# Optimization experiments

Hardware: AMD Instinct MI355X
Metric: run time of the kernel (lower is better)

Reference implementation:

```python
import jax, jax.numpy as jnp
import numpy as np

D_MODEL = 1024
D_STATE = 16
D_CONV = 4
EXPAND = 2
D_INNER = D_MODEL * EXPAND
B_BATCH = 2
SEQ_L = 2048


def setup_inputs() -> dict:
    key = jax.random.key(0)
    ks = jax.random.split(key, 9)
    x = jax.random.normal(ks[0], (B_BATCH, SEQ_L, D_MODEL), dtype=jnp.float32)
    # Parameters (torch nn.Linear stores weight as (out, in))
    in_proj_w = jax.random.normal(ks[1], (2 * D_INNER, D_MODEL), jnp.float32) / np.sqrt(D_MODEL)
    conv_w = jax.random.normal(ks[2], (D_INNER, 1, D_CONV), jnp.float32) / np.sqrt(D_CONV)
    conv_b = jax.random.normal(ks[3], (D_INNER,), jnp.float32) * 0.01
    dt_w = jax.random.normal(ks[4], (D_INNER, D_INNER), jnp.float32) / np.sqrt(D_INNER)
    dt_b = jax.random.uniform(ks[5], (D_INNER,), jnp.float32, 1.0, 2.0)
    B_proj_w = jax.random.normal(ks[6], (D_STATE, D_INNER), jnp.float32) / np.sqrt(D_INNER)
    C_proj_w = jax.random.normal(ks[7], (D_STATE, D_INNER), jnp.float32) / np.sqrt(D_INNER)
    A_log = jnp.broadcast_to(jnp.log(jnp.linspace(1.0, D_STATE, D_STATE, dtype=jnp.float32))[None, :], (D_INNER, D_STATE)).copy()
    D_param = jnp.ones((D_INNER,), jnp.float32)
    out_proj_w = jax.random.normal(ks[8], (D_MODEL, D_INNER), jnp.float32) / np.sqrt(D_INNER)
    return {"x": x, "in_proj_w": in_proj_w, "conv_w": conv_w, "conv_b": conv_b,
            "dt_w": dt_w, "dt_b": dt_b, "B_proj_w": B_proj_w, "C_proj_w": C_proj_w,
            "A_log": A_log, "D_param": D_param, "out_proj_w": out_proj_w}


def reference(x, in_proj_w, conv_w, conv_b, dt_w, dt_b, B_proj_w, C_proj_w, A_log, D_param, out_proj_w):
    Bb, L, _ = x.shape
    # 1. input projection + split into (x_proj, z)
    xz = jnp.einsum('bld,ed->ble', x, in_proj_w)            # (B, L, 2*Din)
    x_p, z = jnp.split(xz, 2, axis=-1)                      # each (B, L, Din)
    # 2. causal depthwise conv1d (left-pad K-1, trim to L == torch pad=K-1 then [:L])
    xc = x_p.transpose(0, 2, 1)                             # (B, Din, L)
    K = conv_w.shape[-1]
    xc = jax.lax.conv_general_dilated(xc, conv_w, window_strides=(1,),
                                      padding=[(K - 1, 0)],
                                      feature_group_count=xc.shape[1])
    xc = xc + conv_b[None, :, None]
    xs = jax.nn.silu(xc).transpose(0, 2, 1)                 # (B, L, Din)
    # 3. SSM parameter projections
    dt = jax.nn.softplus(jnp.einsum('bld,ed->ble', xs, dt_w) + dt_b)  # (B, L, Din)
    Bp = jnp.einsum('bld,nd->bln', xs, B_proj_w)            # (B, L, N)
    Cp = jnp.einsum('bld,nd->bln', xs, C_proj_w)            # (B, L, N)
    A = -jnp.exp(A_log)                                     # (Din, N)
    # 4. selective scan: h[t] = exp(dt*A)*h[t-1] + dt*B*x ; y = <h, C> + D*x
    def step(h, inp):
        dt_t, B_t, x_t, C_t = inp                           # (B,Din),(B,N),(B,Din),(B,N)
        a = jnp.exp(dt_t[..., None] * A)                    # (B, Din, N)
        b = dt_t[..., None] * B_t[:, None, :] * x_t[..., None]
        h = a * h + b
        y_t = jnp.einsum('bdn,bn->bd', h, C_t)
        return h, y_t
    h0 = jnp.zeros((Bb, xs.shape[-1], A.shape[1]), x.dtype)
    scan_in = (dt.transpose(1, 0, 2), Bp.transpose(1, 0, 2),
               xs.transpose(1, 0, 2), Cp.transpose(1, 0, 2))
    _, ys = jax.lax.scan(step, h0, scan_in)                 # (L, B, Din)
    y = ys.transpose(1, 0, 2) + D_param * xs                # (B, L, Din)
    # 5. gated output projection
    y = y * jax.nn.silu(z)
    return jnp.einsum('ble,de->bld', y, out_proj_w)         # (B, L, d_model)
```

## Files before the change

### kernel.cpp

```cpp
#include <hip/hip_runtime.h>
#include <cmath>

#define BB 2
#define LL 2048
#define DMODEL 1024
#define DIN 2048
#define NST 16
#define NC 32
#define TC 64

typedef short short8 __attribute__((ext_vector_type(8)));
typedef float f32x4 __attribute__((ext_vector_type(4)));
typedef unsigned short u16;

__device__ __forceinline__ float bf2f(u16 u) {
    union { unsigned u; float f; } v; v.u = ((unsigned)u) << 16; return v.f;
}
__device__ __forceinline__ u16 f2bf(float f) {
    union { float f; unsigned u; } v; v.f = f;
    unsigned r = v.u + 0x7FFFu + ((v.u >> 16) & 1u);
    return (u16)(r >> 16);
}

__global__ __launch_bounds__(256) void cvt_bf16(const float* __restrict__ in,
                                                u16* __restrict__ out) {
    int i = (blockIdx.x * 256 + threadIdx.x) * 4;
    float4 v = *reinterpret_cast<const float4*>(in + i);
    ushort4 o = {f2bf(v.x), f2bf(v.y), f2bf(v.z), f2bf(v.w)};
    *reinterpret_cast<ushort4*>(out + i) = o;
}

template <int KDIM, int EPI>
__global__ __launch_bounds__(256, 2) void gemm128(const u16* __restrict__ A,
                                                  const u16* __restrict__ B,
                                                  void* __restrict__ Cout, int N,
                                                  const float* __restrict__ bias,
                                                  float* __restrict__ Bp,
                                                  float* __restrict__ Cp) {
    constexpr int NT = KDIM / 64;
    __shared__ u16 lds[32768];
    const int tid = threadIdx.x;
    const int lane = tid & 63;
    const int wave = tid >> 6;
    const int bm = blockIdx.y * 128;
    const int bn = blockIdx.x * 128;
    const int wr = (wave >> 1) * 64;
    const int wc = (wave & 1) * 64;
    const int fr = lane & 15;
    const int kg8 = (lane >> 4) * 8;

    u16* const A0 = lds;
    u16* const B0 = lds + 8192;
    u16* const A1 = lds + 16384;
    u16* const B1 = lds + 24576;

    f32x4 acc[4][4];
#pragma unroll
    for (int i = 0; i < 4; ++i)
#pragma unroll
        for (int j = 0; j < 4; ++j) acc[i][j] = (f32x4){0.f, 0.f, 0.f, 0.f};

    auto STAGE = [&](const u16* __restrict__ G, int br, int kt, u16* dst) {
#pragma unroll
        for (int rr = 0; rr < 4; ++rr) {
            int c = rr * 256 + tid;
            int cs = c ^ ((c >> 4) & 7);
            __builtin_amdgcn_global_load_lds(
                (const __attribute__((address_space(1))) void*)(
                    G + (size_t)(br + (cs >> 3)) * KDIM + kt + ((cs & 7) << 3)),
                (__attribute__((address_space(3))) void*)(dst + c * 8), 16, 0, 0);
        }
    };
    auto LDSW = [&](const u16* tile, int row, int k) -> short8 {
        int u = row * 64 + k;
        u ^= ((u >> 7) & 7) << 3;
        return *reinterpret_cast<const short8*>(tile + u);
    };

    STAGE(A, bm, 0, A0);
    STAGE(B, bn, 0, B0);
    __syncthreads();

#pragma unroll 1
    for (int t = 0; t < NT; ++t) {
        const u16* const Ac = (t & 1) ? A1 : A0;
        const u16* const Bc = (t & 1) ? B1 : B0;
        u16* const An = (t & 1) ? A0 : A1;
        u16* const Bn = (t & 1) ? B0 : B1;

        if (t + 1 < NT) {
            STAGE(A, bm, (t + 1) * 64, An);
            STAGE(B, bn, (t + 1) * 64, Bn);
        }

        short8 af[4][2], bf[4][2];
#pragma unroll
        for (int f = 0; f < 4; ++f)
#pragma unroll
            for (int ks = 0; ks < 2; ++ks)
                af[f][ks] = LDSW(Ac, wr + f * 16 + fr, ks * 32 + kg8);
#pragma unroll
        for (int j = 0; j < 4; ++j)
#pragma unroll
            for (int ks = 0; ks < 2; ++ks)
                bf[j][ks] = LDSW(Bc, wc + j * 16 + fr, ks * 32 + kg8);

#pragma unroll
        for (int ks = 0; ks < 2; ++ks)
#pragma unroll
            for (int f = 0; f < 4; ++f)
#pragma unroll
                for (int j = 0; j < 4; ++j)
                    acc[f][j] = __builtin_amdgcn_mfma_f32_16x16x32_bf16(
                        af[f][ks], bf[j][ks], acc[f][j], 0, 0, 0);

        __syncthreads();
    }

    const int crow0 = (lane >> 4) * 4;
    const int ccol = lane & 15;
#pragma unroll
    for (int f = 0; f < 4; ++f)
#pragma unroll
        for (int j = 0; j < 4; ++j) {
            const int col = bn + wc + j * 16 + ccol;
            if (EPI == 1 && col >= DIN + 32) continue;
            float bv = (EPI == 1 && col < DIN) ? bias[col] : 0.f;
#pragma unroll
            for (int r = 0; r < 4; ++r) {
                const int row = bm + wr + f * 16 + crow0 + r;
                float v = acc[f][j][r];
                if (EPI == 0) {
                    ((float*)Cout)[(size_t)row * N + col] = v;
                } else if (EPI == 2) {
                    ((u16*)Cout)[(size_t)row * N + col] = f2bf(v);
                } else {
                    if (col < DIN) {
                        v += bv;
                        v = (v > 20.0f) ? v : log1pf(__expf(v));
                        ((float*)Cout)[(size_t)row * DIN + col] = v;
                    } else if (col < DIN + 16) {
                        Bp[(size_t)row * NST + (col - DIN)] = v;
                    } else {
                        Cp[(size_t)row * NST + (col - DIN - 16)] = v;
                    }
                }
            }
        }
}

__global__ __launch_bounds__(256) void conv_silu(const u16* __restrict__ xz,
                                                 const float* __restrict__ w,
                                                 const float* __restrict__ b,
                                                 u16* __restrict__ xsb) {
    int idx = blockIdx.x * 256 + threadIdx.x;
    int d = idx & (DIN - 1);
    int t = (idx >> 11) & (LL - 1);
    int bb = idx >> 22;
    const u16* xp = xz + (size_t)bb * LL * 4096;
    float acc = b[d];
#pragma unroll
    for (int k = 0; k < 4; ++k) {
        int tt = t - 3 + k;
        if (tt >= 0) acc = fmaf(w[d * 4 + k], bf2f(xp[(size_t)tt * 4096 + d]), acc);
    }
    float s = acc / (1.0f + __expf(-acc));
    xsb[idx] = f2bf(s);
}

__global__ __launch_bounds__(256) void scan1(const float* __restrict__ dt,
                                             const u16* __restrict__ xs,
                                             const float* __restrict__ Bp,
                                             const float* __restrict__ A_log,
                                             float* __restrict__ aprod,
                                             float* __restrict__ hout) {
    const int db = blockIdx.x & 7;
    const int c = (blockIdx.x >> 3) & (NC - 1);
    const int b = blockIdx.x >> 8;
    const int d = db * 256 + threadIdx.x;
    const int t0 = c * TC;

    __shared__ float Bs[TC * NST];
    for (int i = threadIdx.x; i < TC * NST; i += 256)
        Bs[i] = Bp[((size_t)b * LL + t0) * NST + i];
    __syncthreads();

    float Ac[NST];
#pragma unroll
    for (int n = 0; n < NST; ++n) Ac[n] = -__expf(A_log[d * NST + n]);

    float ap[NST], h[NST];
#pragma unroll
    for (int n = 0; n < NST; ++n) { ap[n] = 1.0f; h[n] = 0.0f; }

    const float* dtp = dt + ((size_t)b * LL + t0) * DIN + d;
    const u16*  xp  = xs + ((size_t)b * LL + t0) * DIN + d;

    for (int tt = 0; tt < TC; ++tt) {
        float dtv = dtp[(size_t)tt * DIN];
        float xv = bf2f(xp[(size_t)tt * DIN]);
        float bx = dtv * xv;
#pragma unroll
        for (int n = 0; n < NST; ++n) {
            float a = __expf(dtv * Ac[n]);
            ap[n] *= a;
            h[n] = fmaf(a, h[n], bx * Bs[tt * NST + n]);
        }
    }
#pragma unroll
    for (int n = 0; n < NST; ++n) {
        size_t idx = (((size_t)(b * NC + c) * NST) + n) * DIN + d;
        aprod[idx] = ap[n];
        hout[idx] = h[n];
    }
}

__global__ __launch_bounds__(256) void scan2(const float* __restrict__ aprod,
                                             const float* __restrict__ hout,
                                             float* __restrict__ hin) {
    const int gid = blockIdx.x * 256 + threadIdx.x;
    const int d = gid & (DIN - 1);
    const int n = (gid >> 11) & (NST - 1);
    const int b = gid >> 15;
    float h = 0.0f;
    for (int c = 0; c < NC; ++c) {
        size_t idx = (((size_t)(b * NC + c) * NST) + n) * DIN + d;
        hin[idx] = h;
        h = fmaf(aprod[idx], h, hout[idx]);
    }
}

__global__ __launch_bounds__(256) void scan3(const float* __restrict__ dt,
                                             const u16* __restrict__ xs,
                                             const u16* __restrict__ xz,
                                             const float* __restrict__ Bp,
                                             const float* __restrict__ Cp,
                                             const float* __restrict__ hin,
                                             const float* __restrict__ A_log,
                                             const float* __restrict__ Dp,
                                             u16* __restrict__ ybf) {
    const int db = blockIdx.x & 7;
    const int c = (blockIdx.x >> 3) & (NC - 1);
    const int b = blockIdx.x >> 8;
    const int d = db * 256 + threadIdx.x;
    const int t0 = c * TC;

    __shared__ float Bs[TC * NST];
    __shared__ float Cs[TC * NST];
    for (int i = threadIdx.x; i < TC * NST; i += 256) {
        Bs[i] = Bp[((size_t)b * LL + t0) * NST + i];
        Cs[i] = Cp[((size_t)b * LL + t0) * NST + i];
    }
    __syncthreads();

    float Ac[NST], h[NST];
#pragma unroll
    for (int n = 0; n < NST; ++n) {
        Ac[n] = -__expf(A_log[d * NST + n]);
        h[n] = hin[(((size_t)(b * NC + c) * NST) + n) * DIN + d];
    }
    const float Dv = Dp[d];

    const float* dtp = dt + ((size_t)b * LL + t0) * DIN + d;
    const u16*  xp  = xs + ((size_t)b * LL + t0) * DIN + d;
    const u16*  zp  = xz + ((size_t)b * LL + t0) * 4096 + DIN + d;
    u16* yp = ybf + ((size_t)b * LL + t0) * DIN + d;

    for (int tt = 0; tt < TC; ++tt) {
        float dtv = dtp[(size_t)tt * DIN];
        float xv = bf2f(xp[(size_t)tt * DIN]);
        float zv = bf2f(zp[(size_t)tt * 4096]);
        float bx = dtv * xv;
        float y = 0.0f;
#pragma unroll
        for (int n = 0; n < NST; ++n) {
            float a = __expf(dtv * Ac[n]);
            h[n] = fmaf(a, h[n], bx * Bs[tt * NST + n]);
            y = fmaf(h[n], Cs[tt * NST + n], y);
        }
        y = fmaf(Dv, xv, y);
        float g = zv / (1.0f + __expf(-zv));
        yp[(size_t)tt * DIN] = f2bf(y * g);
    }
}

extern "C" void kernel_launch(void* const* d_in, const int* in_sizes, int n_in,
                              void* d_out, int out_size, void* d_ws, size_t ws_size,
                              hipStream_t stream) {
    const float* x          = (const float*)d_in[0];
    const float* in_proj_w  = (const float*)d_in[1];
    const float* conv_w     = (const float*)d_in[2];
    const float* conv_b     = (const float*)d_in[3];
    const float* dt_w       = (const float*)d_in[4];
    const float* dt_b       = (const float*)d_in[5];
    const float* B_proj_w   = (const float*)d_in[6];
    const float* C_proj_w   = (const float*)d_in[7];
    const float* A_log      = (const float*)d_in[8];
    const float* D_param    = (const float*)d_in[9];
    const float* out_proj_w = (const float*)d_in[10];
    float* out = (float*)d_out;
    float* ws  = (float*)d_ws;

    float* dtbuf = ws;
    float* Bp    = ws + 8388608;
    float* Cp    = ws + 8454144;
    float* aprod = ws + 8519680;
    float* hout  = ws + 10616832;
    float* hin   = ws + 12713984;
    u16* bfbase   = (u16*)(ws + 14811136);
    u16* x_bf     = bfbase;
    u16* w1_bf    = bfbase + 4194304;
    u16* y_bf     = bfbase;
    u16* xz_bf    = bfbase + 8388608;
    u16* wdtbc_bf = bfbase + 25165824;
    u16* wout_bf  = bfbase + 29622272;
    u16* xs_bf    = bfbase + 31719424;

    const int M = BB * LL;

    cvt_bf16<<<4194304 / 1024, 256, 0, stream>>>(x, x_bf);
    cvt_bf16<<<4194304 / 1024, 256, 0, stream>>>(in_proj_w, w1_bf);
    cvt_bf16<<<4194304 / 1024, 256, 0, stream>>>(dt_w, wdtbc_bf);
    cvt_bf16<<<32768 / 1024, 256, 0, stream>>>(B_proj_w, wdtbc_bf + (size_t)DIN * DIN);
    cvt_bf16<<<32768 / 1024, 256, 0, stream>>>(C_proj_w, wdtbc_bf + (size_t)(DIN + 16) * DIN);
    cvt_bf16<<<2097152 / 1024, 256, 0, stream>>>(out_proj_w, wout_bf);

    gemm128<1024, 2><<<dim3(32, 32), 256, 0, stream>>>(
        x_bf, w1_bf, xz_bf, 4096, nullptr, nullptr, nullptr);

    conv_silu<<<(BB * LL * DIN) / 256, 256, 0, stream>>>(xz_bf, conv_w, conv_b, xs_bf);

    gemm128<2048, 1><<<dim3(17, 32), 256, 0, stream>>>(
        xs_bf, wdtbc_bf, dtbuf, DIN, dt_b, Bp, Cp);

    scan1<<<BB * NC * 8, 256, 0, stream>>>(dtbuf, xs_bf, Bp, A_log, aprod, hout);
    scan2<<<(BB * NST * DIN) / 256, 256, 0, stream>>>(aprod, hout, hin);
    scan3<<<BB * NC * 8, 256, 0, stream>>>(dtbuf, xs_bf, xz_bf, Bp, Cp, hin,
                                           A_log, D_param, y_bf);

    gemm128<2048, 0><<<dim3(8, 32), 256, 0, stream>>>(
        y_bf, wout_bf, out, DMODEL, nullptr, nullptr, nullptr);
}
```

Measured before the change: 437.3 us.

## Merge bf16 conversions into one launch and shrink GEMM K-tile for occupancy

Six separate fp32-to-bf16 conversion launches become a single kernel that picks its source and destination by block index, removing launch overhead. The GEMM K-tile drops from 64 to 32, halving LDS to 32 KB and raising launch_bounds to 4 blocks per CU to gain occupancy. The XOR swizzle on LDS reads and writes is removed, so LDS bank conflicts may appear, and twice as many barrier iterations are needed per GEMM.

```diff
diff --git a/kernel.cpp b/kernel.cpp
--- a/kernel.cpp
+++ b/kernel.cpp
@@ -22,23 +22,39 @@
     return (u16)(r >> 16);
 }
 
-__global__ __launch_bounds__(256) void cvt_bf16(const float* __restrict__ in,
-                                                u16* __restrict__ out) {
-    int i = (blockIdx.x * 256 + threadIdx.x) * 4;
-    float4 v = *reinterpret_cast<const float4*>(in + i);
+__global__ __launch_bounds__(256) void cvt_all(const float* __restrict__ x,
+                                               const float* __restrict__ w1,
+                                               const float* __restrict__ dtw,
+                                               const float* __restrict__ Bw,
+                                               const float* __restrict__ Cw,
+                                               const float* __restrict__ wo,
+                                               u16* __restrict__ x_bf,
+                                               u16* __restrict__ w1_bf,
+                                               u16* __restrict__ wdtbc_bf,
+                                               u16* __restrict__ wout_bf) {
+    int blk = blockIdx.x;
+    const float* src; u16* dst; int off;
+    if (blk < 4096)        { src = x;   dst = x_bf;   off = blk; }
+    else if (blk < 8192)   { src = w1;  dst = w1_bf;  off = blk - 4096; }
+    else if (blk < 12288)  { src = dtw; dst = wdtbc_bf; off = blk - 8192; }
+    else if (blk < 12320)  { src = Bw;  dst = wdtbc_bf + (size_t)DIN * DIN; off = blk - 12288; }
+    else if (blk < 12352)  { src = Cw;  dst = wdtbc_bf + (size_t)(DIN + 16) * DIN; off = blk - 12320; }
+    else                   { src = wo;  dst = wout_bf; off = blk - 12352; }
+    int i = off * 1024 + threadIdx.x * 4;
+    float4 v = *reinterpret_cast<const float4*>(src + i);
     ushort4 o = {f2bf(v.x), f2bf(v.y), f2bf(v.z), f2bf(v.w)};
-    *reinterpret_cast<ushort4*>(out + i) = o;
+    *reinterpret_cast<ushort4*>(dst + i) = o;
 }
 
 template <int KDIM, int EPI>
-__global__ __launch_bounds__(256, 2) void gemm128(const u16* __restrict__ A,
+__global__ __launch_bounds__(256, 4) void gemm128(const u16* __restrict__ A,
                                                   const u16* __restrict__ B,
                                                   void* __restrict__ Cout, int N,
                                                   const float* __restrict__ bias,
                                                   float* __restrict__ Bp,
                                                   float* __restrict__ Cp) {
-    constexpr int NT = KDIM / 64;
-    __shared__ u16 lds[32768];
+    constexpr int NT = KDIM / 32;
+    __shared__ u16 lds[16384];
     const int tid = threadIdx.x;
     const int lane = tid & 63;
     const int wave = tid >> 6;
@@ -50,9 +66,9 @@
     const int kg8 = (lane >> 4) * 8;
 
     u16* const A0 = lds;
-    u16* const B0 = lds + 8192;
-    u16* const A1 = lds + 16384;
-    u16* const B1 = lds + 24576;
+    u16* const B0 = lds + 4096;
+    u16* const A1 = lds + 8192;
+    u16* const B1 = lds + 12288;
 
     f32x4 acc[4][4];
 #pragma unroll
@@ -62,19 +78,13 @@
 
     auto STAGE = [&](const u16* __restrict__ G, int br, int kt, u16* dst) {
 #pragma unroll
-        for (int rr = 0; rr < 4; ++rr) {
+        for (int rr = 0; rr < 2; ++rr) {
             int c = rr * 256 + tid;
-            int cs = c ^ ((c >> 4) & 7);
             __builtin_amdgcn_global_load_lds(
                 (const __attribute__((address_space(1))) void*)(
-                    G + (size_t)(br + (cs >> 3)) * KDIM + kt + ((cs & 7) << 3)),
+                    G + (size_t)(br + (c >> 2)) * KDIM + kt + ((c & 3) << 3)),
                 (__attribute__((address_space(3))) void*)(dst + c * 8), 16, 0, 0);
         }
-    };
-    auto LDSW = [&](const u16* tile, int row, int k) -> short8 {
-        int u = row * 64 + k;
-        u ^= ((u >> 7) & 7) << 3;
-        return *reinterpret_cast<const short8*>(tile + u);
     };
 
     STAGE(A, bm, 0, A0);
@@ -89,30 +99,24 @@
         u16* const Bn = (t & 1) ? B0 : B1;
 
         if (t + 1 < NT) {
-            STAGE(A, bm, (t + 1) * 64, An);
-            STAGE(B, bn, (t + 1) * 64, Bn);
-        }
-
-        short8 af[4][2], bf[4][2];
+            STAGE(A, bm, (t + 1) * 32, An);
+            STAGE(B, bn, (t + 1) * 32, Bn);
+        }
+
+        short8 af[4], bf[4];
 #pragma unroll
         for (int f = 0; f < 4; ++f)
-#pragma unroll
-            for (int ks = 0; ks < 2; ++ks)
-                af[f][ks] = LDSW(Ac, wr + f * 16 + fr, ks * 32 + kg8);
+            af[f] = *reinterpret_cast<const short8*>(Ac + (wr + f * 16 + fr) * 32 + kg8);
 #pragma unroll
         for (int j = 0; j < 4; ++j)
-#pragma unroll
-            for (int ks = 0; ks < 2; ++ks)
-                bf[j][ks] = LDSW(Bc, wc + j * 16 + fr, ks * 32 + kg8);
-
-#pragma unroll
-        for (int ks = 0; ks < 2; ++ks)
-#pragma unroll
-            for (int f = 0; f < 4; ++f)
-#pragma unroll
-                for (int j = 0; j < 4; ++j)
-                    acc[f][j] = __builtin_amdgcn_mfma_f32_16x16x32_bf16(
-                        af[f][ks], bf[j][ks], acc[f][j], 0, 0, 0);
+            bf[j] = *reinterpret_cast<const short8*>(Bc + (wc + j * 16 + fr) * 32 + kg8);
+
+#pragma unroll
+        for (int f = 0; f < 4; ++f)
+#pragma unroll
+            for (int j = 0; j < 4; ++j)
+                acc[f][j] = __builtin_amdgcn_mfma_f32_16x16x32_bf16(
+                    af[f], bf[j], acc[f][j], 0, 0, 0);
 
         __syncthreads();
     }
@@ -318,12 +322,8 @@
 
     const int M = BB * LL;
 
-    cvt_bf16<<<4194304 / 1024, 256, 0, stream>>>(x, x_bf);
-    cvt_bf16<<<4194304 / 1024, 256, 0, stream>>>(in_proj_w, w1_bf);
-    cvt_bf16<<<4194304 / 1024, 256, 0, stream>>>(dt_w, wdtbc_bf);
-    cvt_bf16<<<32768 / 1024, 256, 0, stream>>>(B_proj_w, wdtbc_bf + (size_t)DIN * DIN);
-    cvt_bf16<<<32768 / 1024, 256, 0, stream>>>(C_proj_w, wdtbc_bf + (size_t)(DIN + 16) * DIN);
-    cvt_bf16<<<2097152 / 1024, 256, 0, stream>>>(out_proj_w, wout_bf);
+    cvt_all<<<14400, 256, 0, stream>>>(x, in_proj_w, dt_w, B_proj_w, C_proj_w,
+                                       out_proj_w, x_bf, w1_bf, wdtbc_bf, wout_bf);
 
     gemm128<1024, 2><<<dim3(32, 32), 256, 0, stream>>>(
         x_bf, w1_bf, xz_bf, 4096, nullptr, nullptr, nullptr);
```

Result: faster. 413.3 us (-5.5%).
